# Kernel optimization log

Hardware: AMD Instinct MI355X
Metric: run time of the kernel (lower is better)

Reference implementation:

```python
import jax, jax.numpy as jnp
from jax import lax
import numpy as np

RATE = 2      # dilation/matching rate
KSIZE = 3     # contextual-attention patch size
SCALE = 10.0  # softmax_scale
ESC_NAN = 1e-4


def conv2d(x, w, pad):
    return lax.conv_general_dilated(x, w, (1, 1), ((pad, pad), (pad, pad)),
                                    dimension_numbers=('NCHW', 'OIHW', 'NCHW'))


def extract_patches(x, kernel, stride):
    # torch: ZeroPad2d(1) then x.unfold(2,k,s).unfold(3,k,s) -> [B, C, nH, nW, k, k]
    x = jnp.pad(x, ((0, 0), (0, 0), (1, 1), (1, 1)))
    H, W = x.shape[2], x.shape[3]
    nH = (H - kernel) // stride + 1
    nW = (W - kernel) // stride + 1
    R = jnp.arange(nH)[:, None] * stride + jnp.arange(kernel)[None, :]   # [nH, k]
    Cc = jnp.arange(nW)[:, None] * stride + jnp.arange(kernel)[None, :]  # [nW, k]
    return x[:, :, R[:, None, :, None], Cc[None, :, None, :]]            # [B,C,nH,nW,k,k]


def _forward(f, b, w1, b1, w2, b2):
    B, C, H, W = f.shape
    kernel = 2 * RATE
    # raw background patches; .contiguous().view in torch is a raw row-major reshape
    raw_w = extract_patches(b, kernel, RATE).reshape(B, -1, C, kernel, kernel)  # [B,L,C,4,4]
    # nearest down_sample by 1/rate == strided slicing
    fd = f[:, :, ::RATE, ::RATE]
    bd = b[:, :, ::RATE, ::RATE]
    FH, FW = fd.shape[2], fd.shape[3]
    BH, BW = bd.shape[2], bd.shape[3]
    L = BH * BW
    w = extract_patches(bd, KSIZE, 1).reshape(B, -1, C, KSIZE, KSIZE)  # [B,L,C,3,3]
    fuse_w = jnp.eye(KSIZE, dtype=f.dtype).reshape(1, 1, KSIZE, KSIZE)

    def per_item(xi, wi, raw_wi):
        # xi [C,FH,FW], wi [L,C,3,3], raw_wi [L,C,4,4]
        norm = jnp.sqrt(jnp.sum(wi * wi, axis=(1, 2, 3), keepdims=True))
        wi_n = wi / jnp.maximum(norm, ESC_NAN)
        yi = conv2d(xi[None], wi_n, 1)                      # [1,L,FH,FW] correlation scores
        # fuse: propagate scores along diagonals via identity-kernel convs + axis swaps
        yi = yi.reshape(1, 1, FH * FW, BH * BW)
        yi = conv2d(yi, fuse_w, 1)
        yi = yi.reshape(1, FH, FW, BH, BW).transpose(0, 2, 1, 4, 3)
        yi = yi.reshape(1, 1, FH * FW, BH * BW)
        yi = conv2d(yi, fuse_w, 1)
        yi = yi.reshape(1, FW, FH, BW, BH).transpose(0, 2, 1, 4, 3)  # [1,FH,FW,BH,BW]
        yi = yi.reshape(1, L, FH, FW)
        # mask is None -> mm == 1 everywhere, so masked softmax == plain scaled softmax
        yi = jax.nn.softmax(yi * SCALE, axis=1)
        # conv_transpose2d(yi, raw_wi, stride=rate, padding=1) / 4:
        # = conv(dilate(yi, rate), flip(raw_wi^T), pad = k-1-p = 2)
        wt = jnp.flip(raw_wi.transpose(1, 0, 2, 3), axis=(2, 3))  # [C,L,4,4] OIHW
        out = lax.conv_general_dilated(yi, wt, (1, 1), ((2, 2), (2, 2)),
                                       lhs_dilation=(RATE, RATE),
                                       dimension_numbers=('NCHW', 'OIHW', 'NCHW')) / 4.0
        return out[0]  # [C,H,W]

    y = jax.vmap(per_item)(fd, w, raw_w)  # [B,C,H,W]
    # self.out: two 3x3 convs, no nonlinearity
    out = conv2d(y, w1, 1) + b1[None, :, None, None]
    out = conv2d(out, w2, 1) + b2[None, :, None, None]
    return out


def setup_inputs():
    key = jax.random.key(0)
    ks = jax.random.split(key, 4)
    B, C, H, W = 4, 64, 96, 96
    f = jax.random.normal(ks[0], (B, C, H, W), dtype=jnp.float32)
    b = jax.random.normal(ks[1], (B, C, H, W), dtype=jnp.float32)
    w1 = jax.random.normal(ks[2], (C, C, 3, 3), dtype=jnp.float32) * 0.05
    b1 = jnp.zeros((C,), dtype=jnp.float32)
    w2 = jax.random.normal(ks[3], (C, C, 3, 3), dtype=jnp.float32) * 0.05
    b2 = jnp.zeros((C,), dtype=jnp.float32)
    return {"f": f, "b": b, "w1": w1, "b1": b1, "w2": w2, "b2": b2}


def reference(f, b, w1, b1, w2, b2):
    return _forward(f, b, w1, b1, w2, b2)
```

## Files before the change

### kernel.cpp

```cpp
#include <hip/hip_runtime.h>
#include <stdint.h>


#define YI 5345296ull
typedef __attribute__((ext_vector_type(8))) short short8;
typedef __attribute__((ext_vector_type(8))) _Float16 half8;
typedef __attribute__((ext_vector_type(4))) float f32x4;
typedef __attribute__((ext_vector_type(4), aligned(4))) float f32x4u;
typedef __attribute__((ext_vector_type(4))) short s16x4;

#if defined(__has_builtin)
#if __has_builtin(__builtin_amdgcn_global_load_lds)
#define HAVE_GLL 1
#endif
#endif

#ifdef HAVE_GLL
typedef const __attribute__((address_space(1))) void* gp1_t;
typedef __attribute__((address_space(3))) void* lp3_t;
__device__ __forceinline__ void gl_lds16(const void* g, void* l){
  __builtin_amdgcn_global_load_lds((gp1_t)g, (lp3_t)l, 16, 0, 0);
}
#else
__device__ __forceinline__ void gl_lds16(const void* g, void* l){
  *(short8*)l = *(const short8*)g;
}
#endif

__device__ __forceinline__ float b2f(uint16_t u){
  union { uint32_t i; float f; } v; v.i = ((uint32_t)u) << 16; return v.f;
}
__device__ __forceinline__ uint16_t f2b(float f){
  uint32_t x = __float_as_uint(f);
  uint32_t r = (x + 0x7FFFu + ((x >> 16) & 1u)) >> 16;
  return (uint16_t)r;
}
__device__ __forceinline__ uint16_t f2h(float f){
  union { _Float16 h; uint16_t u; } v; v.h = (_Float16)f; return v.u;
}
__device__ __forceinline__ float h2f(uint16_t u){
  union { uint16_t u; _Float16 h; } v; v.u = u; return (float)v.h;
}
__device__ __forceinline__ int gfun(int x, int d){
  int t = (x % 48) * 48 + (x / 48) + d;
  if ((unsigned)t >= 2304u) return -1;
  return (t % 48) * 48 + (t / 48);
}


__global__ void k_build_wn(const float* __restrict__ bsrc, uint16_t* __restrict__ wn){
  __shared__ uint16_t lds[576];
  int o = blockIdx.x, item = blockIdx.y, c = threadIdx.x;
  int m = o * 64 + c;
  int c0 = m / 2304, rem = m % 2304, i = rem / 48, j = rem % 48;
  const float* bp = bsrc + ((size_t)item * 64 + c0) * 9216;
  float v[9]; float ss = 0.f;
#pragma unroll
  for (int p = 0; p < 3; p++)
#pragma unroll
    for (int q = 0; q < 3; q++){
      int y = i + p - 1, x = j + q - 1;
      float val = 0.f;
      if ((unsigned)y < 48u && (unsigned)x < 48u) val = bp[y * 192 + x * 2];
      v[p * 3 + q] = val; ss += val * val;
    }
#pragma unroll
  for (int off = 32; off > 0; off >>= 1) ss += __shfl_xor(ss, off, 64);
  float inv = 1.f / fmaxf(sqrtf(ss), 1e-4f);
#pragma unroll
  for (int t = 0; t < 9; t++) lds[c * 9 + t] = f2h(v[t] * inv);
  __syncthreads();
  uint32_t* d32 = (uint32_t*)(wn + ((size_t)item * 2304 + o) * 576);
  const uint32_t* s32 = (const uint32_t*)lds;
#pragma unroll
  for (int k = 0; k < 5; k++){
    int idx = k * 64 + c;
    if (idx < 288) d32[idx] = s32[idx];
  }
}

__global__ void k_build_x(const float* __restrict__ fsrc, uint16_t* __restrict__ xb){
  __shared__ uint16_t lds[1152];
  int s = blockIdx.x, item = blockIdx.y, c = threadIdx.x;
  int y = s / 48, x = s % 48;
  const float* fp = fsrc + ((size_t)item * 64 + c) * 9216;
#pragma unroll
  for (int p = 0; p < 3; p++)
#pragma unroll
    for (int q = 0; q < 3; q++){
      int yy = y + p - 1, xx = x + q - 1;
      float val = 0.f;
      if ((unsigned)yy < 48u && (unsigned)xx < 48u) val = fp[yy * 192 + xx * 2];
      uint16_t hi = f2h(val);
      int t = p * 3 + q;
      lds[c * 9 + t] = hi;
      lds[576 + c * 9 + t] = f2h(val - h2f(hi));
    }
  __syncthreads();
  uint32_t* d32 = (uint32_t*)(xb + ((size_t)item * 2304 + s) * 1152);
  const uint32_t* s32 = (const uint32_t*)lds;
#pragma unroll
  for (int k = 0; k < 9; k++){
    int idx = k * 64 + c;
    d32[idx] = s32[idx];
  }
}


__launch_bounds__(256)
__global__ void k_gemm_corr(const uint16_t* __restrict__ A, const uint16_t* __restrict__ B,
                            float* __restrict__ Cd){
  __shared__ __align__(16) uint16_t As1[128 * 32];
  __shared__ __align__(16) uint16_t As2[128 * 32];
  __shared__ __align__(16) uint16_t Bs[128 * 32];
  int blk = blockIdx.x;
  int k8 = blk & 7, idx = blk >> 3;
  int item = k8 >> 1;
  int n0 = ((k8 & 1) * 9 + idx % 9) * 128;
  int m0 = (idx / 9) * 128;
  const uint16_t* Ap = A + (size_t)item * 2304 * 1152;
  const uint16_t* Bp = B + (size_t)item * 2304 * 576;
  int tid = threadIdx.x;
  int wave = tid >> 6, lane = tid & 63, lm = lane & 15, lg = lane >> 4;
  int wy = wave >> 1, wx = wave & 1;
  int swl = (lg ^ ((lm >> 2) & 3)) * 8;
  f32x4 acc[4][4] = {};
  for (int kt = 0; kt < 18; kt++){
    int kb = kt * 32;
#pragma unroll
    for (int c = tid; c < 1536; c += 256){
      int half = c >> 9;
      int cc = c & 511;
      int row = cc >> 2, j = cc & 3;
      int sw = (j ^ ((row >> 2) & 3)) * 8;
      if (half == 0)
        gl_lds16(&Ap[(size_t)(m0 + row) * 1152 + kb + sw], &As1[cc * 8]);
      else if (half == 1)
        gl_lds16(&Ap[(size_t)(m0 + row) * 1152 + 576 + kb + sw], &As2[cc * 8]);
      else
        gl_lds16(&Bp[(size_t)(n0 + row) * 576 + kb + sw], &Bs[cc * 8]);
    }
    __syncthreads();
    half8 af1[4], af2[4], bf[4];
#pragma unroll
    for (int i = 0; i < 4; i++){
      af1[i] = *(const half8*)&As1[(wy * 64 + i * 16 + lm) * 32 + swl];
      af2[i] = *(const half8*)&As2[(wy * 64 + i * 16 + lm) * 32 + swl];
      bf[i]  = *(const half8*)&Bs[(wx * 64 + i * 16 + lm) * 32 + swl];
    }
#pragma unroll
    for (int i = 0; i < 4; i++)
#pragma unroll
      for (int j = 0; j < 4; j++){
        acc[i][j] = __builtin_amdgcn_mfma_f32_16x16x32_f16(af1[i], bf[j], acc[i][j], 0, 0, 0);
        acc[i][j] = __builtin_amdgcn_mfma_f32_16x16x32_f16(af2[i], bf[j], acc[i][j], 0, 0, 0);
      }
    __syncthreads();
  }
  float* Cp = Cd + (size_t)item * YI + 16;
#pragma unroll
  for (int i = 0; i < 4; i++){
    int rb = m0 + wy * 64 + i * 16 + lg * 4;
#pragma unroll
    for (int j = 0; j < 4; j++){
      int cc = n0 + wx * 64 + j * 16 + lm;
#pragma unroll
      for (int r = 0; r < 4; r++)
        Cp[(size_t)(rb + r) * 2320 + cc] = acc[i][j][r];
    }
  }
}


__global__ void k_misc(float* __restrict__ Yt, uint16_t* __restrict__ pt2,
                       uint16_t* __restrict__ ybt2,
                       const float* __restrict__ w1, const float* __restrict__ w2,
                       uint16_t* __restrict__ p1, uint16_t* __restrict__ p2){
  int blk = blockIdx.x, tid = threadIdx.x;
  if (blk < 36){
    int t = blk * 256 + tid;
    int item = t / 2304, row = t % 2304;
    float* yp = Yt + (size_t)item * YI + 16;
    f32x4 z = {};
#pragma unroll
    for (int q = 0; q < 4; q++) *(f32x4*)&yp[(size_t)row * 2320 + 2304 + 4 * q] = z;
    if (row < 16) (Yt + (size_t)item * YI)[row] = 0.f;
  } else if (blk < 820){
    int p = blk - 36;
    int item = p / 196, pp = p % 196;
    int sy, sx;
    if (pp < 50){ sy = 0; sx = pp; }
    else if (pp < 100){ sy = 49; sx = pp - 50; }
    else if (pp < 148){ sy = pp - 99; sx = 0; }
    else { sy = pp - 147; sx = 49; }
    uint16_t* pr = pt2 + ((size_t)item * 2500 + sy * 50 + sx) * 2304;
    short8 z = {};
    for (int c = tid; c < 288; c += 256) *(short8*)&pr[c * 8] = z;
  } else if (blk < 3221){
    size_t i = ((size_t)(blk - 820) * 256 + tid) * 8;
    short8 z = {};
    *(short8*)&ybt2[i] = z;
  } else {
    int i = (blk - 3221) * 256 + tid;
    int co = i / 576, rem = i % 576, ci = rem / 9, t = rem % 9;
    int di = co * 576 + t * 64 + ci;
    p1[di] = f2b(w1[i]); p2[di] = f2b(w2[i]);
  }
}


__global__ void k_fuse_sm(const float* __restrict__ Yt, uint16_t* __restrict__ pt2){
  __shared__ float red[4];
  int bx = blockIdx.x;
  int s = (bx & 7) * 288 + (bx >> 3);
  int item = blockIdx.y, t = threadIdx.x;
  const float* yp = Yt + (size_t)item * YI + 16;
  int rs[3]; rs[0] = gfun(s, -1); rs[1] = s; rs[2] = gfun(s, 1);
  int nact = (t < 64) ? 3 : 2;
  f32x4u v[3];
  for (int u = 0; u < 3; u++){
    f32x4u acc = {0.f, 0.f, 0.f, 0.f};
    if (u < nact){
      int g = t + u * 256;
      int o0 = 4 * g, orr = o0 / 48, oc0 = o0 % 48;
#pragma unroll
      for (int dd = 0; dd < 3; dd++){
        int a0 = rs[dd];
        if (a0 < 0) continue;
        int d = dd - 1;
        int base; f32x4u mv = {1.f, 1.f, 1.f, 1.f};
        if (d == 0) base = o0;
        else {
          int tor = orr + d;
          if ((unsigned)tor < 48u) base = tor * 48 + oc0;
          else if (tor < 0){ base = 2255 + oc0; if (oc0 == 0) mv[0] = 0.f; }
          else { base = oc0 + 1; if (oc0 == 44) mv[3] = 0.f; }
        }
#pragma unroll
        for (int e = -1; e <= 1; e++){
          int a = a0 + e;
          if ((unsigned)a >= 2304u) continue;
          const float* rowp = yp + (size_t)a * 2320;
          f32x4u x = *(const f32x4u*)&rowp[base + e];
          acc += x * mv;
        }
      }
    }
    v[u] = acc;
  }
  float mx = -3.4e38f;
  for (int u = 0; u < nact; u++)
#pragma unroll
    for (int i = 0; i < 4; i++) mx = fmaxf(mx, v[u][i]);
#pragma unroll
  for (int off = 32; off > 0; off >>= 1) mx = fmaxf(mx, __shfl_xor(mx, off, 64));
  if ((t & 63) == 0) red[t >> 6] = mx;
  __syncthreads();
  mx = fmaxf(fmaxf(red[0], red[1]), fmaxf(red[2], red[3]));
  float sum = 0.f;
  for (int u = 0; u < nact; u++)
#pragma unroll
    for (int i = 0; i < 4; i++){ v[u][i] = __expf(10.f * (v[u][i] - mx)); sum += v[u][i]; }
#pragma unroll
  for (int off = 32; off > 0; off >>= 1) sum += __shfl_xor(sum, off, 64);
  __syncthreads();
  if ((t & 63) == 0) red[t >> 6] = sum;
  __syncthreads();
  float inv = 1.f / (red[0] + red[1] + red[2] + red[3]);
  uint16_t* pr = pt2 + ((size_t)item * 2500 + (size_t)(s / 48 + 1) * 50 + (s % 48) + 1) * 2304;
  for (int u = 0; u < nact; u++){
    s16x4 w;
#pragma unroll
    for (int i = 0; i < 4; i++) w[i] = (short)f2b(v[u][i] * inv);
    *(s16x4*)&pr[4 * (t + u * 256)] = w;
  }
}


__global__ void k_build_rwa(const float* __restrict__ bsrc, uint16_t* __restrict__ rwa){
  __shared__ uint16_t tile[64][66];
  int item = blockIdx.y, l0 = blockIdx.x * 64;
  const float* bp = bsrc + (size_t)item * 64 * 9216;
  int wave = threadIdx.x >> 6, lane = threadIdx.x & 63;
  for (int tap = 0; tap < 16; tap++){
    int py = tap >> 2, qx = tap & 3;
#pragma unroll
    for (int step = 0; step < 16; step++){
      int lsub = wave * 16 + step;
      int l = l0 + lsub, co = lane;
      int m = l * 64 + co;
      int c0 = m / 2304, rem = m % 2304, i = rem / 48, jj = rem % 48;
      int Y = 2 * i + py - 1, X = 2 * jj + qx - 1;
      float val = 0.f;
      if ((unsigned)Y < 96u && (unsigned)X < 96u) val = bp[(size_t)c0 * 9216 + Y * 96 + X];
      tile[lsub][co] = f2b(val);
    }
    __syncthreads();
#pragma unroll
    for (int step = 0; step < 16; step++){
      int co = wave * 16 + step;
      rwa[(((size_t)item * 16 + tap) * 64 + co) * 2304 + l0 + lane] = tile[lane][co];
    }
    __syncthreads();
  }
}


__launch_bounds__(256)
__global__ void k_deconv2(const uint16_t* __restrict__ rwa, const uint16_t* __restrict__ pt2,
                          uint16_t* __restrict__ T){
  __shared__ __align__(16) uint16_t As[128 * 64];
  __shared__ __align__(16) uint16_t Bs[128 * 64];
  int blk = blockIdx.x;
  int k8 = blk & 7, idx = blk >> 3;
  int item = k8 >> 1;
  int n0 = ((k8 & 1) * 10 + idx % 10) * 128;
  int m0 = (idx / 10) * 128;
  const uint16_t* Ap = rwa + (size_t)item * 1024 * 2304;
  const uint16_t* Bp = pt2 + (size_t)item * 2500 * 2304;
  int tid = threadIdx.x;
  int wave = tid >> 6, lane = tid & 63, lm = lane & 15, lg = lane >> 4;
  int wy = wave >> 1, wx = wave & 1;
  f32x4 acc[4][4] = {};
  for (int kt = 0; kt < 36; kt++){
    int kb = kt * 64;
#pragma unroll
    for (int c = tid; c < 2048; c += 256){
      int cc = c & 1023;
      int row = cc >> 3, pj = cc & 7;
      int jl = pj ^ (row & 7);
      if (c < 1024)
        gl_lds16(&Ap[(size_t)(m0 + row) * 2304 + kb + jl * 8], &As[cc * 8]);
      else
        gl_lds16(&Bp[(size_t)(n0 + row) * 2304 + kb + jl * 8], &Bs[cc * 8]);
    }
    __syncthreads();
#pragma unroll
    for (int k2 = 0; k2 < 2; k2++){
      short8 af[4], bf[4];
#pragma unroll
      for (int i = 0; i < 4; i++){
        int rowa = wy * 64 + i * 16 + lm;
        int pja = (k2 * 4 + lg) ^ (lm & 7);
        af[i] = *(const short8*)&As[rowa * 64 + pja * 8];
        int rowb = wx * 64 + i * 16 + lm;
        bf[i] = *(const short8*)&Bs[rowb * 64 + pja * 8];
      }
#pragma unroll
      for (int i = 0; i < 4; i++)
#pragma unroll
        for (int j = 0; j < 4; j++)
          acc[i][j] = __builtin_amdgcn_mfma_f32_16x16x32_bf16(af[i], bf[j], acc[i][j], 0, 0, 0);
    }
    __syncthreads();
  }
  uint16_t* Tp = T + (size_t)item * 1024 * 2560;
#pragma unroll
  for (int i = 0; i < 4; i++){
    int rb = m0 + wy * 64 + i * 16 + lg * 4;
#pragma unroll
    for (int j = 0; j < 4; j++){
      int cc = n0 + wx * 64 + j * 16 + lm;
#pragma unroll
      for (int r = 0; r < 4; r++)
        Tp[(size_t)(rb + r) * 2560 + cc] = f2b(acc[i][j][r]);
    }
  }
}

__global__ void k_dred2(const uint16_t* __restrict__ T, uint16_t* __restrict__ ybt2){
  int my = blockIdx.x, phase = blockIdx.y, item = blockIdx.z;
  int co = threadIdx.x;
  int fy = phase >> 1, fx = phase & 1;
  const uint16_t* Tp = T + (size_t)item * 1024 * 2560;
  uint16_t* op = ybt2 + (size_t)item * 98 * 98 * 64;
  for (int mx = 0; mx < 48; mx++){
    float acc = 0.f;
#pragma unroll
    for (int ay = 0; ay < 2; ay++)
#pragma unroll
      for (int ax = 0; ax < 2; ax++){
        int tap = (3 - fy - 2 * ay) * 4 + (3 - fx - 2 * ax);
        int sp = (my + ay + fy) * 50 + (mx + ax + fx);
        acc += b2f(Tp[(size_t)(tap * 64 + co) * 2560 + sp]);
      }
    int Y = 2 * my + fy + 1, X = 2 * mx + fx + 1;
    op[((size_t)Y * 98 + X) * 64 + co] = f2b(acc * 0.25f);
  }
}


__launch_bounds__(256)
__global__ void k_conv_gemm2(const uint16_t* __restrict__ Wp, const uint16_t* __restrict__ Src,
                             const float* __restrict__ bias,
                             uint16_t* __restrict__ dst16, float* __restrict__ dst32){
  __shared__ __align__(16) uint16_t As[64 * 32];
  __shared__ __align__(16) uint16_t Bs[128 * 32];
  int n0 = blockIdx.x * 128, item = blockIdx.z;
  int tid = threadIdx.x, wave = tid >> 6, lane = tid & 63, lm = lane & 15, lg = lane >> 4;
  int swl = (lg ^ ((lm >> 2) & 3)) * 8;
  const uint16_t* Bp = Src + (size_t)item * 98 * 98 * 64;
  f32x4 acc[4][2] = {};
  for (int kt = 0; kt < 18; kt++){
    int t = kt >> 1, cb = (kt & 1) * 32;
    int py = t / 3, qx = t % 3;
#pragma unroll
    for (int c = tid; c < 768; c += 256){
      if (c < 256){
        int row = c >> 2, j = c & 3;
        int sw = (j ^ ((row >> 2) & 3)) * 8;
        gl_lds16(&Wp[(size_t)row * 576 + kt * 32 + sw], &As[c * 8]);
      } else {
        int cc = c - 256; int row = cc >> 2, j = cc & 3;
        int sw = (j ^ ((row >> 2) & 3)) * 8;
        int n = n0 + row; int y = n / 96, x = n % 96;
        gl_lds16(&Bp[((size_t)(y + py) * 98 + (x + qx)) * 64 + cb + sw], &Bs[cc * 8]);
      }
    }
    __syncthreads();
    short8 af[4], bf[2];
#pragma unroll
    for (int i = 0; i < 4; i++) af[i] = *(const short8*)&As[(i * 16 + lm) * 32 + swl];
#pragma unroll
    for (int j = 0; j < 2; j++) bf[j] = *(const short8*)&Bs[(wave * 32 + j * 16 + lm) * 32 + swl];
#pragma unroll
    for (int i = 0; i < 4; i++)
#pragma unroll
      for (int j = 0; j < 2; j++)
        acc[i][j] = __builtin_amdgcn_mfma_f32_16x16x32_bf16(af[i], bf[j], acc[i][j], 0, 0, 0);
    __syncthreads();
  }
  if (dst32){
#pragma unroll
    for (int i = 0; i < 4; i++)
#pragma unroll
      for (int j = 0; j < 2; j++){
        int n = n0 + wave * 32 + j * 16 + lm;
#pragma unroll
        for (int r = 0; r < 4; r++){
          int co = i * 16 + lg * 4 + r;
          dst32[((size_t)item * 64 + co) * 9216 + n] = acc[i][j][r] + bias[co];
        }
      }
  } else {
    uint16_t* dp = dst16 + (size_t)item * 98 * 98 * 64;
#pragma unroll
    for (int i = 0; i < 4; i++)
#pragma unroll
      for (int j = 0; j < 2; j++){
        int n = n0 + wave * 32 + j * 16 + lm;
        int y = n / 96, x = n % 96;
        int co0 = i * 16 + lg * 4;
        s16x4 w;
#pragma unroll
        for (int r = 0; r < 4; r++) w[r] = (short)f2b(acc[i][j][r] + bias[co0 + r]);
        *(s16x4*)&dp[((size_t)(y + 1) * 98 + (x + 1)) * 64 + co0] = w;
      }
  }
}


extern "C" void kernel_launch(void* const* d_in, const int* in_sizes, int n_in,
                              void* d_out, int out_size, void* d_ws, size_t ws_size,
                              hipStream_t stream){
  const float* f  = (const float*)d_in[0];
  const float* b  = (const float*)d_in[1];
  const float* w1 = (const float*)d_in[2];
  const float* b1 = (const float*)d_in[3];
  const float* w2 = (const float*)d_in[4];
  const float* b2 = (const float*)d_in[5];
  char* ws = (char*)d_ws;
  float*    Yt   = (float*)ws;
  uint16_t* Wn   = (uint16_t*)(ws + 85524736ull);
  uint16_t* Xb   = (uint16_t*)(ws + 96141568ull);
  uint16_t* Pt2  = (uint16_t*)(ws + 85524736ull);
  uint16_t* Rwa  = (uint16_t*)(ws + 131604736ull);
  uint16_t* Ybt2 = (uint16_t*)(ws + 150479104ull);
  uint16_t* Y1t2 = (uint16_t*)(ws + 155396352ull);
  uint16_t* Wp1  = (uint16_t*)(ws + 160313600ull);
  uint16_t* Wp2  = (uint16_t*)(ws + 160387328ull);
  uint16_t* T    = (uint16_t*)ws;
  float*    out  = (float*)d_out;

  k_build_wn<<<dim3(2304, 4), 64, 0, stream>>>(b, Wn);
  k_build_x<<<dim3(2304, 4), 64, 0, stream>>>(f, Xb);
  k_gemm_corr<<<dim3(1296), 256, 0, stream>>>(Xb, Wn, Yt);
  k_misc<<<dim3(3365), 256, 0, stream>>>(Yt, Pt2, Ybt2, w1, w2, Wp1, Wp2);
  k_build_rwa<<<dim3(36, 4), 256, 0, stream>>>(b, Rwa);
  k_fuse_sm<<<dim3(2304, 4), 256, 0, stream>>>(Yt, Pt2);
  k_deconv2<<<dim3(640), 256, 0, stream>>>(Rwa, Pt2, T);
  k_dred2<<<dim3(48, 4, 4), 64, 0, stream>>>(T, Ybt2);
  k_conv_gemm2<<<dim3(72, 1, 4), 256, 0, stream>>>(Wp1, Ybt2, b1, Y1t2, nullptr);
  k_conv_gemm2<<<dim3(72, 1, 4), 256, 0, stream>>>(Wp2, Y1t2, b2, nullptr, out);
}
```

Baseline: 369.0 us.

## Merge prep kernels, fold pad zeroing into fuse_sm, transpose T, widen conv K-tile

Folds the separate build_wn, build_x, build_rwa and misc-init kernels into one launch of 256-thread blocks, each handling four items, and moves the Pt2 border zeroing into extra blocks of k_fuse_sm. This removes several launches and the tiny 64-thread blocks. The deconv output T is now stored transposed with packed 4-wide bf16 stores, so k_dred2 reads along contiguous channels. k_conv_gemm2 loads a 64-wide K slab per tap with an 8-way XOR swizzle, halving its barrier count. The catch is more LDS per block and branchy combined kernels.

```diff
diff --git a/kernel.cpp b/kernel.cpp
--- a/kernel.cpp
+++ b/kernel.cpp
@@ -48,61 +48,111 @@
 }
 
 
-__global__ void k_build_wn(const float* __restrict__ bsrc, uint16_t* __restrict__ wn){
-  __shared__ uint16_t lds[576];
-  int o = blockIdx.x, item = blockIdx.y, c = threadIdx.x;
-  int m = o * 64 + c;
-  int c0 = m / 2304, rem = m % 2304, i = rem / 48, j = rem % 48;
-  const float* bp = bsrc + ((size_t)item * 64 + c0) * 9216;
-  float v[9]; float ss = 0.f;
-#pragma unroll
-  for (int p = 0; p < 3; p++)
-#pragma unroll
-    for (int q = 0; q < 3; q++){
-      int y = i + p - 1, x = j + q - 1;
-      float val = 0.f;
-      if ((unsigned)y < 48u && (unsigned)x < 48u) val = bp[y * 192 + x * 2];
-      v[p * 3 + q] = val; ss += val * val;
-    }
-#pragma unroll
-  for (int off = 32; off > 0; off >>= 1) ss += __shfl_xor(ss, off, 64);
-  float inv = 1.f / fmaxf(sqrtf(ss), 1e-4f);
-#pragma unroll
-  for (int t = 0; t < 9; t++) lds[c * 9 + t] = f2h(v[t] * inv);
-  __syncthreads();
-  uint32_t* d32 = (uint32_t*)(wn + ((size_t)item * 2304 + o) * 576);
-  const uint32_t* s32 = (const uint32_t*)lds;
-#pragma unroll
-  for (int k = 0; k < 5; k++){
-    int idx = k * 64 + c;
-    if (idx < 288) d32[idx] = s32[idx];
-  }
-}
-
-__global__ void k_build_x(const float* __restrict__ fsrc, uint16_t* __restrict__ xb){
-  __shared__ uint16_t lds[1152];
-  int s = blockIdx.x, item = blockIdx.y, c = threadIdx.x;
-  int y = s / 48, x = s % 48;
-  const float* fp = fsrc + ((size_t)item * 64 + c) * 9216;
-#pragma unroll
-  for (int p = 0; p < 3; p++)
-#pragma unroll
-    for (int q = 0; q < 3; q++){
-      int yy = y + p - 1, xx = x + q - 1;
-      float val = 0.f;
-      if ((unsigned)yy < 48u && (unsigned)xx < 48u) val = fp[yy * 192 + xx * 2];
-      uint16_t hi = f2h(val);
-      int t = p * 3 + q;
-      lds[c * 9 + t] = hi;
-      lds[576 + c * 9 + t] = f2h(val - h2f(hi));
-    }
-  __syncthreads();
-  uint32_t* d32 = (uint32_t*)(xb + ((size_t)item * 2304 + s) * 1152);
-  const uint32_t* s32 = (const uint32_t*)lds;
-#pragma unroll
-  for (int k = 0; k < 9; k++){
-    int idx = k * 64 + c;
-    d32[idx] = s32[idx];
+__global__ void k_build(const float* __restrict__ fsrc, const float* __restrict__ bsrc,
+                        uint16_t* __restrict__ wn, uint16_t* __restrict__ xb,
+                        uint16_t* __restrict__ rwa, float* __restrict__ Yt,
+                        uint16_t* __restrict__ ybt2,
+                        const float* __restrict__ w1, const float* __restrict__ w2,
+                        uint16_t* __restrict__ p1, uint16_t* __restrict__ p2){
+  __shared__ __align__(16) uint16_t shm[4608];
+  int blk = blockIdx.x, tid = threadIdx.x;
+  if (blk < 2304){
+    int p = blk * 4 + (tid >> 6), c = tid & 63;
+    int o = p % 2304, item = p / 2304;
+    int m = o * 64 + c;
+    int c0 = m / 2304, rem = m % 2304, i = rem / 48, j = rem % 48;
+    const float* bp = bsrc + ((size_t)item * 64 + c0) * 9216;
+    float v[9]; float ss = 0.f;
+#pragma unroll
+    for (int pp = 0; pp < 3; pp++)
+#pragma unroll
+      for (int q = 0; q < 3; q++){
+        int y = i + pp - 1, x = j + q - 1;
+        float val = 0.f;
+        if ((unsigned)y < 48u && (unsigned)x < 48u) val = bp[y * 192 + x * 2];
+        v[pp * 3 + q] = val; ss += val * val;
+      }
+#pragma unroll
+    for (int off = 32; off > 0; off >>= 1) ss += __shfl_xor(ss, off, 64);
+    float inv = 1.f / fmaxf(sqrtf(ss), 1e-4f);
+    uint16_t* lds = &shm[(tid >> 6) * 576];
+#pragma unroll
+    for (int t = 0; t < 9; t++) lds[c * 9 + t] = f2h(v[t] * inv);
+    __syncthreads();
+    uint32_t* d32 = (uint32_t*)(wn + ((size_t)item * 2304 + o) * 576);
+    const uint32_t* s32 = (const uint32_t*)lds;
+#pragma unroll
+    for (int k = 0; k < 5; k++){
+      int idx = k * 64 + c;
+      if (idx < 288) d32[idx] = s32[idx];
+    }
+  } else if (blk < 4608){
+    int p = (blk - 2304) * 4 + (tid >> 6), c = tid & 63;
+    int s = p % 2304, item = p / 2304;
+    int y = s / 48, x = s % 48;
+    const float* fp = fsrc + ((size_t)item * 64 + c) * 9216;
+    uint16_t* lds = &shm[(tid >> 6) * 1152];
+#pragma unroll
+    for (int pp = 0; pp < 3; pp++)
+#pragma unroll
+      for (int q = 0; q < 3; q++){
+        int yy = y + pp - 1, xx = x + q - 1;
+        float val = 0.f;
+        if ((unsigned)yy < 48u && (unsigned)xx < 48u) val = fp[yy * 192 + xx * 2];
+        uint16_t hi = f2h(val);
+        int t = pp * 3 + q;
+        lds[c * 9 + t] = hi;
+        lds[576 + c * 9 + t] = f2h(val - h2f(hi));
+      }
+    __syncthreads();
+    uint32_t* d32 = (uint32_t*)(xb + ((size_t)item * 2304 + s) * 1152);
+    const uint32_t* s32 = (const uint32_t*)lds;
+#pragma unroll
+    for (int k = 0; k < 9; k++) d32[k * 64 + c] = s32[k * 64 + c];
+  } else if (blk < 4752){
+    uint16_t (*tile)[66] = (uint16_t(*)[66])shm;
+    int bb = blk - 4608;
+    int item = bb / 36, l0 = (bb % 36) * 64;
+    const float* bp = bsrc + (size_t)item * 64 * 9216;
+    int wave = tid >> 6, lane = tid & 63;
+    for (int tap = 0; tap < 16; tap++){
+      int py = tap >> 2, qx = tap & 3;
+#pragma unroll
+      for (int step = 0; step < 16; step++){
+        int lsub = wave * 16 + step;
+        int l = l0 + lsub, co = lane;
+        int m = l * 64 + co;
+        int c0 = m / 2304, rem = m % 2304, i = rem / 48, jj = rem % 48;
+        int Y = 2 * i + py - 1, X = 2 * jj + qx - 1;
+        float val = 0.f;
+        if ((unsigned)Y < 96u && (unsigned)X < 96u) val = bp[(size_t)c0 * 9216 + Y * 96 + X];
+        tile[lsub][co] = f2b(val);
+      }
+      __syncthreads();
+#pragma unroll
+      for (int step = 0; step < 16; step++){
+        int co = wave * 16 + step;
+        rwa[(((size_t)item * 16 + tap) * 64 + co) * 2304 + l0 + lane] = tile[lane][co];
+      }
+      __syncthreads();
+    }
+  } else if (blk < 4788){
+    int t = (blk - 4752) * 256 + tid;
+    int item = t / 2304, row = t % 2304;
+    float* yp = Yt + (size_t)item * YI + 16;
+    f32x4 z = {};
+#pragma unroll
+    for (int q = 0; q < 4; q++) *(f32x4*)&yp[(size_t)row * 2320 + 2304 + 4 * q] = z;
+    if (row < 16) (Yt + (size_t)item * YI)[row] = 0.f;
+  } else if (blk < 7189){
+    size_t i = ((size_t)(blk - 4788) * 256 + tid) * 8;
+    short8 z = {};
+    *(short8*)&ybt2[i] = z;
+  } else {
+    int i = (blk - 7189) * 256 + tid;
+    int co = i / 576, rem = i % 576, ci = rem / 9, t = rem % 9;
+    int di = co * 576 + t * 64 + ci;
+    p1[di] = f2b(w1[i]); p2[di] = f2b(w2[i]);
   }
 }
 
@@ -172,22 +222,12 @@
 }
 
 
-__global__ void k_misc(float* __restrict__ Yt, uint16_t* __restrict__ pt2,
-                       uint16_t* __restrict__ ybt2,
-                       const float* __restrict__ w1, const float* __restrict__ w2,
-                       uint16_t* __restrict__ p1, uint16_t* __restrict__ p2){
-  int blk = blockIdx.x, tid = threadIdx.x;
-  if (blk < 36){
-    int t = blk * 256 + tid;
-    int item = t / 2304, row = t % 2304;
-    float* yp = Yt + (size_t)item * YI + 16;
-    f32x4 z = {};
-#pragma unroll
-    for (int q = 0; q < 4; q++) *(f32x4*)&yp[(size_t)row * 2320 + 2304 + 4 * q] = z;
-    if (row < 16) (Yt + (size_t)item * YI)[row] = 0.f;
-  } else if (blk < 820){
-    int p = blk - 36;
-    int item = p / 196, pp = p % 196;
+__global__ void k_fuse_sm(const float* __restrict__ Yt, uint16_t* __restrict__ pt2){
+  __shared__ float red[4];
+  int bx = blockIdx.x;
+  int item = blockIdx.y, t = threadIdx.x;
+  if (bx >= 2304){
+    int pp = bx - 2304;
     int sy, sx;
     if (pp < 50){ sy = 0; sx = pp; }
     else if (pp < 100){ sy = 49; sx = pp - 50; }
@@ -195,25 +235,10 @@
     else { sy = pp - 147; sx = 49; }
     uint16_t* pr = pt2 + ((size_t)item * 2500 + sy * 50 + sx) * 2304;
     short8 z = {};
-    for (int c = tid; c < 288; c += 256) *(short8*)&pr[c * 8] = z;
-  } else if (blk < 3221){
-    size_t i = ((size_t)(blk - 820) * 256 + tid) * 8;
-    short8 z = {};
-    *(short8*)&ybt2[i] = z;
-  } else {
-    int i = (blk - 3221) * 256 + tid;
-    int co = i / 576, rem = i % 576, ci = rem / 9, t = rem % 9;
-    int di = co * 576 + t * 64 + ci;
-    p1[di] = f2b(w1[i]); p2[di] = f2b(w2[i]);
-  }
-}
-
-
-__global__ void k_fuse_sm(const float* __restrict__ Yt, uint16_t* __restrict__ pt2){
-  __shared__ float red[4];
-  int bx = blockIdx.x;
+    for (int c = t; c < 288; c += 256) *(short8*)&pr[c * 8] = z;
+    return;
+  }
   int s = (bx & 7) * 288 + (bx >> 3);
-  int item = blockIdx.y, t = threadIdx.x;
   const float* yp = Yt + (size_t)item * YI + 16;
   int rs[3]; rs[0] = gfun(s, -1); rs[1] = s; rs[2] = gfun(s, 1);
   int nact = (t < 64) ? 3 : 2;
@@ -273,35 +298,6 @@
 #pragma unroll
     for (int i = 0; i < 4; i++) w[i] = (short)f2b(v[u][i] * inv);
     *(s16x4*)&pr[4 * (t + u * 256)] = w;
-  }
-}
-
-
-__global__ void k_build_rwa(const float* __restrict__ bsrc, uint16_t* __restrict__ rwa){
-  __shared__ uint16_t tile[64][66];
-  int item = blockIdx.y, l0 = blockIdx.x * 64;
-  const float* bp = bsrc + (size_t)item * 64 * 9216;
-  int wave = threadIdx.x >> 6, lane = threadIdx.x & 63;
-  for (int tap = 0; tap < 16; tap++){
-    int py = tap >> 2, qx = tap & 3;
-#pragma unroll
-    for (int step = 0; step < 16; step++){
-      int lsub = wave * 16 + step;
-      int l = l0 + lsub, co = lane;
-      int m = l * 64 + co;
-      int c0 = m / 2304, rem = m % 2304, i = rem / 48, jj = rem % 48;
-      int Y = 2 * i + py - 1, X = 2 * jj + qx - 1;
-      float val = 0.f;
-      if ((unsigned)Y < 96u && (unsigned)X < 96u) val = bp[(size_t)c0 * 9216 + Y * 96 + X];
-      tile[lsub][co] = f2b(val);
-    }
-    __syncthreads();
-#pragma unroll
-    for (int step = 0; step < 16; step++){
-      int co = wave * 16 + step;
-      rwa[(((size_t)item * 16 + tap) * 64 + co) * 2304 + l0 + lane] = tile[lane][co];
-    }
-    __syncthreads();
   }
 }
 
@@ -354,16 +350,17 @@
     }
     __syncthreads();
   }
-  uint16_t* Tp = T + (size_t)item * 1024 * 2560;
+  uint16_t* Tp = T + (size_t)item * 2560 * 1024;
 #pragma unroll
   for (int i = 0; i < 4; i++){
     int rb = m0 + wy * 64 + i * 16 + lg * 4;
 #pragma unroll
     for (int j = 0; j < 4; j++){
       int cc = n0 + wx * 64 + j * 16 + lm;
-#pragma unroll
-      for (int r = 0; r < 4; r++)
-        Tp[(size_t)(rb + r) * 2560 + cc] = f2b(acc[i][j][r]);
+      s16x4 w;
+#pragma unroll
+      for (int r = 0; r < 4; r++) w[r] = (short)f2b(acc[i][j][r]);
+      *(s16x4*)&Tp[(size_t)cc * 1024 + rb] = w;
     }
   }
 }
@@ -372,7 +369,7 @@
   int my = blockIdx.x, phase = blockIdx.y, item = blockIdx.z;
   int co = threadIdx.x;
   int fy = phase >> 1, fx = phase & 1;
-  const uint16_t* Tp = T + (size_t)item * 1024 * 2560;
+  const uint16_t* Tp = T + (size_t)item * 2560 * 1024;
   uint16_t* op = ybt2 + (size_t)item * 98 * 98 * 64;
   for (int mx = 0; mx < 48; mx++){
     float acc = 0.f;
@@ -382,7 +379,7 @@
       for (int ax = 0; ax < 2; ax++){
         int tap = (3 - fy - 2 * ay) * 4 + (3 - fx - 2 * ax);
         int sp = (my + ay + fy) * 50 + (mx + ax + fx);
-        acc += b2f(Tp[(size_t)(tap * 64 + co) * 2560 + sp]);
+        acc += b2f(Tp[(size_t)sp * 1024 + tap * 64 + co]);
       }
     int Y = 2 * my + fy + 1, X = 2 * mx + fx + 1;
     op[((size_t)Y * 98 + X) * 64 + co] = f2b(acc * 0.25f);
@@ -394,40 +391,42 @@
 __global__ void k_conv_gemm2(const uint16_t* __restrict__ Wp, const uint16_t* __restrict__ Src,
                              const float* __restrict__ bias,
                              uint16_t* __restrict__ dst16, float* __restrict__ dst32){
-  __shared__ __align__(16) uint16_t As[64 * 32];
-  __shared__ __align__(16) uint16_t Bs[128 * 32];
+  __shared__ __align__(16) uint16_t As[64 * 64];
+  __shared__ __align__(16) uint16_t Bs[128 * 64];
   int n0 = blockIdx.x * 128, item = blockIdx.z;
   int tid = threadIdx.x, wave = tid >> 6, lane = tid & 63, lm = lane & 15, lg = lane >> 4;
-  int swl = (lg ^ ((lm >> 2) & 3)) * 8;
   const uint16_t* Bp = Src + (size_t)item * 98 * 98 * 64;
   f32x4 acc[4][2] = {};
-  for (int kt = 0; kt < 18; kt++){
-    int t = kt >> 1, cb = (kt & 1) * 32;
+  for (int t = 0; t < 9; t++){
     int py = t / 3, qx = t % 3;
 #pragma unroll
-    for (int c = tid; c < 768; c += 256){
-      if (c < 256){
-        int row = c >> 2, j = c & 3;
-        int sw = (j ^ ((row >> 2) & 3)) * 8;
-        gl_lds16(&Wp[(size_t)row * 576 + kt * 32 + sw], &As[c * 8]);
+    for (int c = tid; c < 1536; c += 256){
+      if (c < 512){
+        int row = c >> 3, pj = c & 7;
+        int jl = pj ^ (row & 7);
+        gl_lds16(&Wp[(size_t)row * 576 + t * 64 + jl * 8], &As[c * 8]);
       } else {
-        int cc = c - 256; int row = cc >> 2, j = cc & 3;
-        int sw = (j ^ ((row >> 2) & 3)) * 8;
+        int cc = c - 512; int row = cc >> 3, pj = cc & 7;
+        int jl = pj ^ (row & 7);
         int n = n0 + row; int y = n / 96, x = n % 96;
-        gl_lds16(&Bp[((size_t)(y + py) * 98 + (x + qx)) * 64 + cb + sw], &Bs[cc * 8]);
-      }
-    }
-    __syncthreads();
-    short8 af[4], bf[2];
-#pragma unroll
-    for (int i = 0; i < 4; i++) af[i] = *(const short8*)&As[(i * 16 + lm) * 32 + swl];
-#pragma unroll
-    for (int j = 0; j < 2; j++) bf[j] = *(const short8*)&Bs[(wave * 32 + j * 16 + lm) * 32 + swl];
-#pragma unroll
-    for (int i = 0; i < 4; i++)
-#pragma unroll
-      for (int j = 0; j < 2; j++)
-        acc[i][j] = __builtin_amdgcn_mfma_f32_16x16x32_bf16(af[i], bf[j], acc[i][j], 0, 0, 0);
+        gl_lds16(&Bp[((size_t)(y + py) * 98 + (x + qx)) * 64 + jl * 8], &Bs[cc * 8]);
+      }
+    }
+    __syncthreads();
+#pragma unroll
+    for (int k2 = 0; k2 < 2; k2++){
+      short8 af[4], bf[2];
+      int pja = (k2 * 4 + lg) ^ (lm & 7);
+#pragma unroll
+      for (int i = 0; i < 4; i++) af[i] = *(const short8*)&As[(i * 16 + lm) * 64 + pja * 8];
+#pragma unroll
+      for (int j = 0; j < 2; j++) bf[j] = *(const short8*)&Bs[(wave * 32 + j * 16 + lm) * 64 + pja * 8];
+#pragma unroll
+      for (int i = 0; i < 4; i++)
+#pragma unroll
+        for (int j = 0; j < 2; j++)
+          acc[i][j] = __builtin_amdgcn_mfma_f32_16x16x32_bf16(af[i], bf[j], acc[i][j], 0, 0, 0);
+    }
     __syncthreads();
   }
   if (dst32){
@@ -482,12 +481,9 @@
   uint16_t* T    = (uint16_t*)ws;
   float*    out  = (float*)d_out;
 
-  k_build_wn<<<dim3(2304, 4), 64, 0, stream>>>(b, Wn);
-  k_build_x<<<dim3(2304, 4), 64, 0, stream>>>(f, Xb);
+  k_build<<<dim3(7333), 256, 0, stream>>>(f, b, Wn, Xb, Rwa, Yt, Ybt2, w1, w2, Wp1, Wp2);
   k_gemm_corr<<<dim3(1296), 256, 0, stream>>>(Xb, Wn, Yt);
-  k_misc<<<dim3(3365), 256, 0, stream>>>(Yt, Pt2, Ybt2, w1, w2, Wp1, Wp2);
-  k_build_rwa<<<dim3(36, 4), 256, 0, stream>>>(b, Rwa);
-  k_fuse_sm<<<dim3(2304, 4), 256, 0, stream>>>(Yt, Pt2);
+  k_fuse_sm<<<dim3(2500, 4), 256, 0, stream>>>(Yt, Pt2);
   k_deconv2<<<dim3(640), 256, 0, stream>>>(Rwa, Pt2, T);
   k_dred2<<<dim3(48, 4, 4), 64, 0, stream>>>(T, Ybt2);
   k_conv_gemm2<<<dim3(72, 1, 4), 256, 0, stream>>>(Wp1, Ybt2, b1, Y1t2, nullptr);
```

Result: faster. 344.7 us (-6.6%).
